# Kernel optimization log

Hardware: AMD Instinct MI355X
Metric: run time of the kernel (lower is better)

## Reference

```python
import jax, jax.numpy as jnp
import numpy as np

B, T, D, K = 4, 2048, 1024, 4

def setup_inputs() -> dict:
    key = jax.random.key(0)
    ks = jax.random.split(key, 4)
    u = jax.random.normal(ks[0], (B, T, D), dtype=jnp.float32)
    s0 = jnp.zeros((B, K, D), dtype=jnp.float32)
    W_in = jax.random.normal(ks[1], (K * D, D), dtype=jnp.float32) * (1.0 / np.sqrt(D))
    b_in = jnp.zeros((K * D,), dtype=jnp.float32)
    W_out = jax.random.normal(ks[2], (D, K * D), dtype=jnp.float32) * (1.0 / np.sqrt(K * D))
    b_out = jnp.zeros((D,), dtype=jnp.float32)
    decay_logit = jax.random.normal(ks[3], (K,), dtype=jnp.float32)
    return {"u": u, "s0": s0, "W_in": W_in, "b_in": b_in,
            "W_out": W_out, "b_out": b_out, "decay_logit": decay_logit}

def reference(u, s0, W_in, b_in, W_out, b_out, decay_logit):
    # u: (B,T,D); s0: (B,K,D)
    Bb, Tt, Dd = u.shape
    Kk = decay_logit.shape[0]
    # input projection -> (B,T,K,D) -> (T,B,K,D) for scan over time
    inp = (jnp.einsum('btd,ed->bte', u, W_in) + b_in).reshape(Bb, Tt, Kk, Dd)
    xs = jnp.transpose(inp, (1, 0, 2, 3))  # (T,B,K,D)
    decay = jax.nn.sigmoid(decay_logit).reshape(1, Kk, 1)  # (1,K,1)

    def step(s, x):
        s_next = decay * s + x
        return s_next, s_next

    s_last, s_seq = jax.lax.scan(step, s0, xs)  # s_seq: (T,B,K,D)
    g_in = jnp.transpose(s_seq, (1, 0, 2, 3)).reshape(Bb, Tt, Kk * Dd)
    g = jnp.einsum('bte,de->btd', g_in, W_out) + b_out
    return g, s_last
```

## Files before the change

kernel.cpp:

```cpp
#include <hip/hip_runtime.h>


#define Bb 4
#define Tt 2048
#define Dd 1024
#define Kk 4
#define BT (Bb*Tt)
#define Ee (Kk*Dd)
#define NCH 32
#define LCH 64

typedef __bf16 bf16x8 __attribute__((ext_vector_type(8)));
typedef float  f32x4  __attribute__((ext_vector_type(4)));

__device__ __forceinline__ float bf2f(ushort u){
  union { unsigned int i; float f; } x; x.i = ((unsigned int)u) << 16; return x.f;
}
__device__ __forceinline__ ushort f2bf(float f){
  union { unsigned int i; float f; } x; x.f = f;
  unsigned int i = x.i;
  return (ushort)((i + 0x7FFFu + ((i >> 16) & 1u)) >> 16);
}
__device__ __forceinline__ float sigm(float x){ return 1.0f / (1.0f + expf(-x)); }

__global__ __launch_bounds__(256) void k_f2bf4(const float4* __restrict__ in,
                                               ushort4* __restrict__ out, int n4){
  int i = blockIdx.x * 256 + threadIdx.x;
  if (i < n4){
    float4 v = in[i];
    ushort4 o; o.x = f2bf(v.x); o.y = f2bf(v.y); o.z = f2bf(v.z); o.w = f2bf(v.w);
    out[i] = o;
  }
}

__global__ __launch_bounds__(256) void k_transpose(const float* __restrict__ in,
                                                   ushort* __restrict__ out){
  __shared__ float tile[32][33];
  int tx = threadIdx.x, ty = threadIdx.y;
  int c0 = blockIdx.x * 32, r0 = blockIdx.y * 32;
  #pragma unroll
  for (int j = 0; j < 4; ++j)
    tile[ty + j*8][tx] = in[(size_t)(r0 + ty + j*8) * Dd + c0 + tx];
  __syncthreads();
  #pragma unroll
  for (int j = 0; j < 4; ++j)
    out[(size_t)(c0 + ty + j*8) * Ee + r0 + tx] = f2bf(tile[tx][ty + j*8]);
}

__global__ __launch_bounds__(256) void gemm_nt(const ushort* __restrict__ A,
                                               const ushort* __restrict__ B,
                                               ushort* __restrict__ C,
                                               int Kred, int lda, int ldb, int ldc,
                                               long aBatch, long bBatch, long cBatch){
  __shared__ ushort As[128 * 32];
  __shared__ ushort Bs[128 * 32];
  A += (long)blockIdx.z * aBatch;
  B += (long)blockIdx.z * bBatch;
  C += (long)blockIdx.z * cBatch;
  const int tid  = threadIdx.x;
  const int lane = tid & 63;
  const int w    = tid >> 6;
  const int wr   = w >> 1, wc = w & 1;
  const int rowBase = blockIdx.x * 128;
  const int colBase = blockIdx.y * 128;

  f32x4 acc[4][4] = {};
  const int krow = (lane >> 4) * 8;
  const int rsel = lane & 15;

  for (int kk = 0; kk < Kred; kk += 32){
    __syncthreads();
    #pragma unroll
    for (int i = 0; i < 2; ++i){
      int c  = i * 256 + tid;
      int r  = c >> 2;
      int c8 = (c & 3) * 8;
      const ushort* ga = A + (size_t)(rowBase + r) * lda + kk + c8;
      const ushort* gb = B + (size_t)(colBase + r) * ldb + kk + c8;
      __builtin_amdgcn_global_load_lds((const __attribute__((address_space(1))) void*)ga,
                                       (__attribute__((address_space(3))) void*)&As[c * 8],
                                       16, 0, 0);
      __builtin_amdgcn_global_load_lds((const __attribute__((address_space(1))) void*)gb,
                                       (__attribute__((address_space(3))) void*)&Bs[c * 8],
                                       16, 0, 0);
    }
    asm volatile("s_waitcnt vmcnt(0)" ::: "memory");
    __syncthreads();

    bf16x8 Af[4], Bf[4];
    #pragma unroll
    for (int mi = 0; mi < 4; ++mi)
      Af[mi] = *(const bf16x8*)&As[(wr*64 + mi*16 + rsel) * 32 + krow];
    #pragma unroll
    for (int ni = 0; ni < 4; ++ni)
      Bf[ni] = *(const bf16x8*)&Bs[(wc*64 + ni*16 + rsel) * 32 + krow];
    #pragma unroll
    for (int mi = 0; mi < 4; ++mi)
      #pragma unroll
      for (int ni = 0; ni < 4; ++ni)
        acc[mi][ni] = __builtin_amdgcn_mfma_f32_16x16x32_bf16(Af[mi], Bf[ni], acc[mi][ni], 0, 0, 0);
  }

  #pragma unroll
  for (int mi = 0; mi < 4; ++mi){
    #pragma unroll
    for (int ni = 0; ni < 4; ++ni){
      int r0 = rowBase + wr*64 + mi*16 + (lane >> 4) * 4;
      int c0 = colBase + wc*64 + ni*16 + (lane & 15);
      #pragma unroll
      for (int q = 0; q < 4; ++q)
        C[(size_t)(r0 + q) * ldc + c0] = f2bf(acc[mi][ni][q]);
    }
  }
}

#define STAGE_HALF(GB, LOFF)                                                   \
  { _Pragma("unroll")                                                          \
    for (int i_ = 0; i_ < 2; ++i_){                                            \
      int c_ = tid + i_*512;                                                   \
      int row_ = c_ >> 2;                                                      \
      int ss_ = (c_ & 3) ^ ((row_ >> 2) & 3);                                  \
      const ushort* g_ = (GB) + (size_t)row_ * 1024 + ss_ * 8;                 \
      __builtin_amdgcn_global_load_lds(                                        \
        (const __attribute__((address_space(1))) void*)g_,                     \
        (__attribute__((address_space(3))) void*)&lds[(LOFF) + c_*8],          \
        16, 0, 0);                                                             \
    } }

#define LDA_H(KH, MH)                                                          \
  { _Pragma("unroll")                                                          \
    for (int mi_ = 0; mi_ < 4; ++mi_){                                         \
      int r_ = wm*128 + (MH)*64 + mi_*16 + rsel;                               \
      int uo_ = r_*32 + kq*8;                                                  \
      uo_ ^= ((uo_ >> 7) & 3) << 3;                                            \
      af[mi_] = *(const bf16x8*)&lds[cbase + (KH)*8192 + uo_];                 \
    } }

#define LDB_ALL(KH)                                                            \
  { _Pragma("unroll")                                                          \
    for (int ni_ = 0; ni_ < 4; ++ni_){                                         \
      int r_ = wn*64 + ni_*16 + rsel;                                          \
      int uo_ = r_*32 + kq*8;                                                  \
      uo_ ^= ((uo_ >> 7) & 3) << 3;                                            \
      bfr[ni_] = *(const bf16x8*)&lds[cbase + 16384 + (KH)*8192 + uo_];        \
    } }

#define WAIT_LGKM()                                                            \
  { asm volatile("s_waitcnt lgkmcnt(0)" ::: "memory");                         \
    __builtin_amdgcn_sched_barrier(0); }

#define MFMA_Q(MH)                                                             \
  { __builtin_amdgcn_s_setprio(1);                                             \
    _Pragma("unroll")                                                          \
    for (int mi_ = 0; mi_ < 4; ++mi_)                                          \
      { _Pragma("unroll")                                                      \
        for (int ni_ = 0; ni_ < 4; ++ni_)                                      \
          acc[(MH)*4+mi_][ni_] = __builtin_amdgcn_mfma_f32_16x16x32_bf16(      \
              af[mi_], bfr[ni_], acc[(MH)*4+mi_][ni_], 0, 0, 0); }             \
    __builtin_amdgcn_s_setprio(0); }

#define BAR() __builtin_amdgcn_s_barrier()

__global__ __launch_bounds__(512, 2) void gemm_big(const ushort* __restrict__ A,
                                                   const ushort* __restrict__ B,
                                                   ushort* __restrict__ C,
                                                   const float* __restrict__ dlog,
                                                   float* __restrict__ carry){
  __shared__ ushort lds[65536];
  const int tid  = threadIdx.x;
  const int lane = tid & 63;
  const int w    = tid >> 6;
  const int wm   = w >> 2;
  const int wn   = w & 3;
  const int rsel = lane & 15;
  const int kq   = lane >> 4;

  int bid = blockIdx.x;
  int xcd = bid & 7, rr = bid >> 3;
  const int rowBase = (((xcd >> 1) << 3) + (rr & 7)) * 256;
  const int colBase = (((xcd & 1) << 3) + (rr >> 3)) * 256;

  const ushort* Ag = A + (size_t)rowBase * 1024;
  const ushort* Bg = B + (size_t)colBase * 1024;

  f32x4 acc[8][4] = {};
  bf16x8 af[4], bfr[4];

  STAGE_HALF(Ag +  0, 0);
  STAGE_HALF(Bg +  0, 16384);
  STAGE_HALF(Ag + 32, 8192);
  STAGE_HALF(Bg + 32, 24576);
  STAGE_HALF(Ag + 64, 32768 + 0);
  STAGE_HALF(Bg + 64, 32768 + 16384);
  asm volatile("s_waitcnt vmcnt(0)" ::: "memory");
  BAR();

  for (int t = 0; t < 16; ++t){
    const int cbase = (t & 1) * 32768;
    const int obase = cbase ^ 32768;
    LDA_H(0, 0); LDB_ALL(0);
    if (t < 15) STAGE_HALF(Ag + (t+1)*64 + 32, obase + 8192);
    BAR();
    WAIT_LGKM();
    MFMA_Q(0);
    BAR();
    LDA_H(0, 1);
    if (t < 15) STAGE_HALF(Bg + (t+1)*64 + 32, obase + 24576);
    BAR();
    WAIT_LGKM();
    MFMA_Q(1);
    if (t < 15) { asm volatile("s_waitcnt vmcnt(6)" ::: "memory"); }
    else        { asm volatile("s_waitcnt vmcnt(0)" ::: "memory"); }
    BAR();
    LDA_H(1, 0); LDB_ALL(1);
    if (t < 14) STAGE_HALF(Ag + (t+2)*64, cbase + 0);
    BAR();
    WAIT_LGKM();
    MFMA_Q(0);
    BAR();
    LDA_H(1, 1);
    if (t < 14) STAGE_HALF(Bg + (t+2)*64, cbase + 16384);
    BAR();
    WAIT_LGKM();
    MFMA_Q(1);
    if (t < 14) { asm volatile("s_waitcnt vmcnt(6)" ::: "memory"); }
    else        { asm volatile("s_waitcnt vmcnt(0)" ::: "memory"); }
    BAR();
  }

  #pragma unroll
  for (int mi = 0; mi < 8; ++mi){
    #pragma unroll
    for (int j = 0; j < 4; ++j){
      #pragma unroll
      for (int q = 0; q < 4; ++q){
        int row = wm*128 + mi*16 + (lane >> 4)*4 + q;
        int col = wn*64 + j*16 + rsel;
        int byte = row*512 + col*2;
        byte ^= ((row >> 2) & 3) << 5;
        *(ushort*)((char*)lds + byte) = f2bf(acc[mi][j][q]);
      }
    }
  }
  __syncthreads();

  {
    const int k_blk = colBase >> 10;
    const int b_blk = rowBase >> 11;
    const int ch0   = (rowBase & 2047) >> 6;
    const int d0    = colBase & 1023;
    const float p   = sigm(dlog[k_blk]);
    #pragma unroll
    for (int s = 0; s < 2; ++s){
      int task = tid + s*512;
      int col = task & 255, ch = task >> 8;
      float a = 0.f;
      for (int i = 0; i < 64; ++i){
        int row = ch*64 + i;
        int byte = row*512 + col*2;
        byte ^= ((row >> 2) & 3) << 5;
        a = p * a + bf2f(*(const ushort*)((char*)lds + byte));
      }
      carry[(size_t)((b_blk*Kk + k_blk)*NCH + ch0 + ch) * Dd + d0 + col] = a;
    }
  }

  #pragma unroll
  for (int j = 0; j < 16; ++j){
    int idx = tid + j*512;
    int r = idx >> 5, c8 = idx & 31;
    int byte = r*512 + c8*16;
    byte ^= ((r >> 2) & 3) << 5;
    f32x4 v = *(const f32x4*)((char*)lds + byte);
    *(f32x4*)&C[(size_t)(rowBase + r) * Ee + colBase + c8*8] = v;
  }
}

__global__ __launch_bounds__(256) void k_z0(const float* __restrict__ Wout,
                                            const float* __restrict__ s0,
                                            float* __restrict__ z0){
  int gid  = blockIdx.x * 4 + (threadIdx.x >> 6);
  int lane = threadIdx.x & 63;
  int d = gid & 1023, k = (gid >> 10) & 3, b = gid >> 12;
  const float* wrow = Wout + (size_t)d * Ee + k * Dd;
  const float* sv   = s0 + ((size_t)(b*Kk + k) << 10);
  float s = 0.f;
  #pragma unroll
  for (int j = 0; j < 16; ++j) s += wrow[lane + j*64] * sv[lane + j*64];
  for (int off = 32; off; off >>= 1) s += __shfl_down(s, off);
  if (lane == 0) z0[gid] = s;
}

__global__ __launch_bounds__(256) void k_cterm(const float* __restrict__ Wout,
                                               const float* __restrict__ b_in,
                                               float* __restrict__ cterm){
  int gid  = blockIdx.x * 4 + (threadIdx.x >> 6);
  int lane = threadIdx.x & 63;
  int d = gid & 1023, k = gid >> 10;
  const float* wrow = Wout + (size_t)d * Ee + k * Dd;
  const float* bv   = b_in + k * Dd;
  float s = 0.f;
  #pragma unroll
  for (int j = 0; j < 16; ++j) s += wrow[lane + j*64] * bv[lane + j*64];
  for (int off = 32; off; off >>= 1) s += __shfl_down(s, off);
  if (lane == 0) cterm[gid] = s;
}

__global__ __launch_bounds__(256) void k_scanInc(const float* __restrict__ carry,
                                                 const float* __restrict__ z0,
                                                 const float* __restrict__ dlog,
                                                 float* __restrict__ incoming){
  int idx = blockIdx.x * 256 + threadIdx.x;
  int k = (idx >> 10) & 3;
  int bk = idx >> 10, d = idx & 1023;
  float p  = sigm(dlog[k]);
  float dL = powf(p, (float)LCH);
  float inc = z0[idx];
  for (int c = 0; c < NCH; ++c){
    size_t o = ((size_t)(bk * NCH + c)) * Dd + d;
    incoming[o] = inc;
    inc = dL * inc + carry[o];
  }
}

__global__ __launch_bounds__(256) void k_scanB(const ushort* __restrict__ Y,
                                               const float* __restrict__ incoming,
                                               const float* __restrict__ dlog,
                                               const float* __restrict__ b_out,
                                               const float* __restrict__ cterm,
                                               float* __restrict__ g){
  int x = blockIdx.x;
  int d = blockIdx.y * 256 + threadIdx.x;
  int c = x & 31, b = x >> 5;
  float p[4], z[4], ct[4], pw[4];
  #pragma unroll
  for (int k = 0; k < 4; ++k){
    p[k]  = sigm(dlog[k]);
    z[k]  = incoming[((size_t)(((b*Kk + k))*NCH + c)) * Dd + d];
    float omp = fmaxf(1.0f - p[k], 1e-30f);
    ct[k] = cterm[k * Dd + d] / omp;
    pw[k] = powf(p[k], (float)(c * LCH + 1));
  }
  float bo = b_out[d];
  size_t ybase = ((size_t)(b*Tt + c*LCH)) * Ee + d;
  size_t gbase = ((size_t)(b*Tt + c*LCH)) * Dd + d;
  for (int i = 0; i < LCH; ++i){
    float acc = bo;
    #pragma unroll
    for (int k = 0; k < 4; ++k){
      z[k] = p[k] * z[k] + bf2f(Y[ybase + (size_t)k * Dd]);
      acc += z[k] + ct[k] * (1.0f - pw[k]);
      pw[k] *= p[k];
    }
    g[gbase] = acc;
    ybase += Ee; gbase += Dd;
  }
}

__global__ __launch_bounds__(256) void k_prep(const float* __restrict__ u,
                                              const float* __restrict__ dlog,
                                              float* __restrict__ vpart,
                                              ushort* __restrict__ U_bf){
  int x = blockIdx.x;
  int d = blockIdx.y * 256 + threadIdx.x;
  int c = x & 31, b = x >> 5;
  float p[4], a[4] = {0.f, 0.f, 0.f, 0.f};
  #pragma unroll
  for (int k = 0; k < 4; ++k) p[k] = sigm(dlog[k]);
  size_t ub = ((size_t)(b*Tt + c*LCH)) * Dd + d;
  for (int i = 0; i < LCH; ++i){
    float uv = u[ub];
    U_bf[ub] = f2bf(uv);
    #pragma unroll
    for (int k = 0; k < 4; ++k) a[k] = p[k] * a[k] + uv;
    ub += Dd;
  }
  #pragma unroll
  for (int k = 0; k < 4; ++k)
    vpart[(((size_t)x) * Kk + k) * Dd + d] = a[k];
}

__global__ __launch_bounds__(256) void k_vcomb(const float* __restrict__ vpart,
                                               const float* __restrict__ dlog,
                                               float* __restrict__ vfull){
  int idx = blockIdx.x * 256 + threadIdx.x;
  int k = (idx >> 10) & 3, b = idx >> 12, d = idx & 1023;
  float p  = sigm(dlog[k]);
  float dL = powf(p, (float)LCH);
  float v = 0.f;
  for (int c = 0; c < NCH; ++c)
    v = dL * v + vpart[(((size_t)(b*NCH + c)) * Kk + k) * Dd + d];
  vfull[idx] = v;
}

__global__ __launch_bounds__(256) void k_slast(const float* __restrict__ W_in,
                                               const float* __restrict__ vfull,
                                               const float* __restrict__ s0,
                                               const float* __restrict__ b_in,
                                               const float* __restrict__ dlog,
                                               float* __restrict__ out){
  int gid  = blockIdx.x * 4 + (threadIdx.x >> 6);
  int lane = threadIdx.x & 63;
  int d = gid & 1023, k = (gid >> 10) & 3, b = gid >> 12;
  const float* wrow = W_in + (size_t)(k*Dd + d) * Dd;
  const float* vv   = vfull + ((size_t)(b*Kk + k) << 10);
  float s = 0.f;
  #pragma unroll
  for (int j = 0; j < 16; ++j) s += wrow[lane + j*64] * vv[lane + j*64];
  for (int off = 32; off; off >>= 1) s += __shfl_down(s, off);
  if (lane == 0){
    float p  = sigm(dlog[k]);
    float pT = powf(p, (float)Tt);
    float omp = 1.0f - p;
    float geo = (omp < 1e-12f) ? (float)Tt : (1.0f - pT) / omp;
    out[gid] = pT * s0[gid] + s + b_in[k*Dd + d] * geo;
  }
}

extern "C" void kernel_launch(void* const* d_in, const int* in_sizes, int n_in,
                              void* d_out, int out_size, void* d_ws, size_t ws_size,
                              hipStream_t stream){
  const float* u     = (const float*)d_in[0];
  const float* s0    = (const float*)d_in[1];
  const float* W_in  = (const float*)d_in[2];
  const float* b_in  = (const float*)d_in[3];
  const float* W_out = (const float*)d_in[4];
  const float* b_out = (const float*)d_in[5];
  const float* dlog  = (const float*)d_in[6];

  float* g_out     = (float*)d_out;
  float* slast_out = g_out + (size_t)BT * Dd;

  char* ws = (char*)d_ws;
  if (ws_size < 115490816ull) return;
  ushort* U_bf    = (ushort*)(ws);
  ushort* WinT    = (ushort*)(ws + 16777216);
  ushort* Wout_bf = (ushort*)(ws + 25165824);
  ushort* Mcat    = (ushort*)(ws + 33554432);
  ushort* Y       = (ushort*)(ws + 41943040);
  float*  carry   = (float*)(ws + 109051904);
  float*  incoming= (float*)(ws + 111149056);
  float*  z0buf   = (float*)(ws + 113246208);
  float*  cterm   = (float*)(ws + 113311744);
  float*  vpart   = (float*)(ws + 113328128);
  float*  vfull   = (float*)(ws + 115425280);

  k_prep<<<dim3(128, 4), 256, 0, stream>>>(u, dlog, vpart, U_bf);
  k_f2bf4<<<4096, 256, 0, stream>>>((const float4*)W_out, (ushort4*)Wout_bf, Dd*Ee/4);
  k_transpose<<<dim3(32, 128), dim3(32, 8), 0, stream>>>(W_in, WinT);

  gemm_nt<<<dim3(8, 8, 4), 256, 0, stream>>>(Wout_bf, WinT, Mcat,
                                             1024, Ee, Ee, Dd,
                                             1024L, 1024L, 1048576L);
  gemm_big<<<512, 512, 0, stream>>>(U_bf, Mcat, Y, dlog, carry);

  k_z0<<<4096, 256, 0, stream>>>(W_out, s0, z0buf);
  k_cterm<<<1024, 256, 0, stream>>>(W_out, b_in, cterm);

  k_scanInc<<<64, 256, 0, stream>>>(carry, z0buf, dlog, incoming);
  k_scanB<<<dim3(128, 4), 256, 0, stream>>>(Y, incoming, dlog, b_out, cterm, g_out);

  k_vcomb<<<64, 256, 0, stream>>>(vpart, dlog, vfull);
  k_slast<<<4096, 256, 0, stream>>>(W_in, vfull, s0, b_in, dlog, slast_out);
}
```

Before: 170.7 us.

## Restructure GEMM main loop to full-tile double buffering with fewer barriers

The big GEMM main loop drops its fine-grained half-tile staging, which used four barrier-separated MFMA quarters per iteration. It now prefetches two full 64-wide K tiles up front and loads all A/B fragments for a tile into separate registers before issuing the MFMAs. Each iteration then waits once, syncs, and issues the next tile's global-to-LDS loads, with two barriers instead of eight. This cuts barrier and waitcnt overhead but keeps more fragments live in registers, removes the setprio hints, and no longer overlaps in-flight LDS stores with the current compute quarter.

```diff
diff --git a/kernel.cpp b/kernel.cpp
--- a/kernel.cpp
+++ b/kernel.cpp
@@ -127,37 +127,31 @@
         16, 0, 0);                                                             \
     } }
 
-#define LDA_H(KH, MH)                                                          \
+#define LOAD_A4(DST, KH, MH)                                                   \
   { _Pragma("unroll")                                                          \
     for (int mi_ = 0; mi_ < 4; ++mi_){                                         \
       int r_ = wm*128 + (MH)*64 + mi_*16 + rsel;                               \
       int uo_ = r_*32 + kq*8;                                                  \
       uo_ ^= ((uo_ >> 7) & 3) << 3;                                            \
-      af[mi_] = *(const bf16x8*)&lds[cbase + (KH)*8192 + uo_];                 \
+      DST[mi_] = *(const bf16x8*)&lds[cbase + (KH)*8192 + uo_];                \
     } }
 
-#define LDB_ALL(KH)                                                            \
+#define LOAD_B4(DST, KH)                                                       \
   { _Pragma("unroll")                                                          \
     for (int ni_ = 0; ni_ < 4; ++ni_){                                         \
       int r_ = wn*64 + ni_*16 + rsel;                                          \
       int uo_ = r_*32 + kq*8;                                                  \
       uo_ ^= ((uo_ >> 7) & 3) << 3;                                            \
-      bfr[ni_] = *(const bf16x8*)&lds[cbase + 16384 + (KH)*8192 + uo_];        \
+      DST[ni_] = *(const bf16x8*)&lds[cbase + 16384 + (KH)*8192 + uo_];        \
     } }
 
-#define WAIT_LGKM()                                                            \
-  { asm volatile("s_waitcnt lgkmcnt(0)" ::: "memory");                         \
-    __builtin_amdgcn_sched_barrier(0); }
-
-#define MFMA_Q(MH)                                                             \
-  { __builtin_amdgcn_s_setprio(1);                                             \
-    _Pragma("unroll")                                                          \
+#define MFMA16(MH, AARR, BARR)                                                 \
+  { _Pragma("unroll")                                                          \
     for (int mi_ = 0; mi_ < 4; ++mi_)                                          \
       { _Pragma("unroll")                                                      \
         for (int ni_ = 0; ni_ < 4; ++ni_)                                      \
           acc[(MH)*4+mi_][ni_] = __builtin_amdgcn_mfma_f32_16x16x32_bf16(      \
-              af[mi_], bfr[ni_], acc[(MH)*4+mi_][ni_], 0, 0, 0); }             \
-    __builtin_amdgcn_s_setprio(0); }
+              AARR[mi_], BARR[ni_], acc[(MH)*4+mi_][ni_], 0, 0, 0); } }
 
 #define BAR() __builtin_amdgcn_s_barrier()
 
@@ -184,7 +178,6 @@
   const ushort* Bg = B + (size_t)colBase * 1024;
 
   f32x4 acc[8][4] = {};
-  bf16x8 af[4], bfr[4];
 
   STAGE_HALF(Ag +  0, 0);
   STAGE_HALF(Bg +  0, 16384);
@@ -192,39 +185,31 @@
   STAGE_HALF(Bg + 32, 24576);
   STAGE_HALF(Ag + 64, 32768 + 0);
   STAGE_HALF(Bg + 64, 32768 + 16384);
-  asm volatile("s_waitcnt vmcnt(0)" ::: "memory");
+  STAGE_HALF(Ag + 96, 32768 + 8192);
+  STAGE_HALF(Bg + 96, 32768 + 24576);
+  asm volatile("s_waitcnt vmcnt(8)" ::: "memory");
   BAR();
 
   for (int t = 0; t < 16; ++t){
     const int cbase = (t & 1) * 32768;
-    const int obase = cbase ^ 32768;
-    LDA_H(0, 0); LDB_ALL(0);
-    if (t < 15) STAGE_HALF(Ag + (t+1)*64 + 32, obase + 8192);
+    bf16x8 am0[4], am1[4], bf0[4];
+    LOAD_A4(am0, 0, 0); LOAD_B4(bf0, 0); LOAD_A4(am1, 0, 1);
+    MFMA16(0, am0, bf0);
+    MFMA16(1, am1, bf0);
+    LOAD_A4(am0, 1, 0); LOAD_B4(bf0, 1); LOAD_A4(am1, 1, 1);
+    MFMA16(0, am0, bf0);
+    MFMA16(1, am1, bf0);
+    asm volatile("s_waitcnt lgkmcnt(0)" ::: "memory");
     BAR();
-    WAIT_LGKM();
-    MFMA_Q(0);
-    BAR();
-    LDA_H(0, 1);
-    if (t < 15) STAGE_HALF(Bg + (t+1)*64 + 32, obase + 24576);
-    BAR();
-    WAIT_LGKM();
-    MFMA_Q(1);
-    if (t < 15) { asm volatile("s_waitcnt vmcnt(6)" ::: "memory"); }
-    else        { asm volatile("s_waitcnt vmcnt(0)" ::: "memory"); }
-    BAR();
-    LDA_H(1, 0); LDB_ALL(1);
-    if (t < 14) STAGE_HALF(Ag + (t+2)*64, cbase + 0);
-    BAR();
-    WAIT_LGKM();
-    MFMA_Q(0);
-    BAR();
-    LDA_H(1, 1);
-    if (t < 14) STAGE_HALF(Bg + (t+2)*64, cbase + 16384);
-    BAR();
-    WAIT_LGKM();
-    MFMA_Q(1);
-    if (t < 14) { asm volatile("s_waitcnt vmcnt(6)" ::: "memory"); }
-    else        { asm volatile("s_waitcnt vmcnt(0)" ::: "memory"); }
+    if (t < 14){
+      STAGE_HALF(Ag + (t+2)*64,      cbase + 0);
+      STAGE_HALF(Bg + (t+2)*64,      cbase + 16384);
+      STAGE_HALF(Ag + (t+2)*64 + 32, cbase + 8192);
+      STAGE_HALF(Bg + (t+2)*64 + 32, cbase + 24576);
+      asm volatile("s_waitcnt vmcnt(8)" ::: "memory");
+    } else {
+      asm volatile("s_waitcnt vmcnt(0)" ::: "memory");
+    }
     BAR();
   }
 
```

Result: no change. 169.4 us (-0.8%).
